# Optimization experiments

Hardware: AMD Instinct MI355X
Metric: run time of the kernel (lower is better)

The kernel has to match this reference:

```python
import jax, jax.numpy as jnp
import numpy as np

B, H = 65536, 1024


def setup_inputs() -> dict:
    key = jax.random.key(0)
    ks = jax.random.split(key, 8)
    pos = jax.random.normal(ks[0], (B, 3), dtype=jnp.float32)
    quat = jax.random.normal(ks[1], (B, 4), dtype=jnp.float32)
    quat = quat / jnp.linalg.norm(quat, axis=-1, keepdims=True)
    gripper = jax.random.randint(ks[2], (B, 1), 0, 2).astype(jnp.float32)
    actions = jnp.concatenate([pos, quat, gripper], axis=-1)  # (B, 8)
    return {
        "actions": actions,
        "pos_W": jax.random.normal(ks[3], (3, H), dtype=jnp.float32) * 0.02,
        "pos_b": jnp.zeros((H,), dtype=jnp.float32),
        "rot_W": jax.random.normal(ks[4], (6, H), dtype=jnp.float32) * 0.02,
        "rot_b": jnp.zeros((H,), dtype=jnp.float32),
        "open_emb": jax.random.normal(ks[5], (2, H), dtype=jnp.float32) * 0.02,
        "ln_g": jnp.ones((H,), dtype=jnp.float32),
        "ln_b": jnp.zeros((H,), dtype=jnp.float32),
    }


def quat_to_euler_xyz(quat):
    # scipy R.from_quat uses (x, y, z, w); as_euler('xyz') = extrinsic x-y-z
    # (classic roll/pitch/yaw). Normalize like scipy does.
    quat = quat / jnp.linalg.norm(quat, axis=-1, keepdims=True)
    x, y, z, w = quat[..., 0], quat[..., 1], quat[..., 2], quat[..., 3]
    roll = jnp.arctan2(2.0 * (w * x + y * z), 1.0 - 2.0 * (x * x + y * y))
    pitch = jnp.arcsin(jnp.clip(2.0 * (w * y - z * x), -1.0, 1.0))
    yaw = jnp.arctan2(2.0 * (w * z + x * y), 1.0 - 2.0 * (y * y + z * z))
    return jnp.stack([roll, pitch, yaw], axis=-1)


def reference(actions, pos_W, pos_b, rot_W, rot_b, open_emb, ln_g, ln_b):
    pos_embeds = actions[..., :3] @ pos_W + pos_b
    open_idx = actions[..., 7].astype(jnp.int32)
    open_embeds = open_emb[open_idx]
    # original detaches quats (.data.cpu()) before conversion
    eul = quat_to_euler_xyz(jax.lax.stop_gradient(actions[..., 3:7]))
    rot_inputs = jnp.concatenate([jnp.sin(eul), jnp.cos(eul)], axis=-1)  # (B, 6)
    rot_embeds = rot_inputs @ rot_W + rot_b
    h = pos_embeds + rot_embeds + open_embeds
    mu = jnp.mean(h, axis=-1, keepdims=True)
    var = jnp.mean(jnp.square(h - mu), axis=-1, keepdims=True)
    return (h - mu) / jnp.sqrt(var + 1e-12) * ln_g + ln_b
```

## Files before the change

kernel.cpp:

```cpp
#include <hip/hip_runtime.h>
#include <math.h>


#define HDIM  1024
#define TPB   256
#define CPT   4
#define RPB   32
#define BATCH 4

typedef float v4f __attribute__((ext_vector_type(4)));

__global__ __launch_bounds__(TPB, 4) void action_embed_kernel(
    const float* __restrict__ actions,
    const float* __restrict__ pos_W, const float* __restrict__ pos_b,
    const float* __restrict__ rot_W, const float* __restrict__ rot_b,
    const float* __restrict__ open_emb,
    const float* __restrict__ ln_g, const float* __restrict__ ln_b,
    float* __restrict__ out, int B)
{
    __shared__ float s_coef[RPB][10];
    __shared__ float s_red[2][BATCH][4][2];

    const int tid  = threadIdx.x;
    const int col  = tid * CPT;
    const int row0 = blockIdx.x * RPB;

    const float4 wp0 = *(const float4*)(pos_W + 0 * HDIM + col);
    const float4 wp1 = *(const float4*)(pos_W + 1 * HDIM + col);
    const float4 wp2 = *(const float4*)(pos_W + 2 * HDIM + col);
    const float4 wr0 = *(const float4*)(rot_W + 0 * HDIM + col);
    const float4 wr1 = *(const float4*)(rot_W + 1 * HDIM + col);
    const float4 wr2 = *(const float4*)(rot_W + 2 * HDIM + col);
    const float4 wr3 = *(const float4*)(rot_W + 3 * HDIM + col);
    const float4 wr4 = *(const float4*)(rot_W + 4 * HDIM + col);
    const float4 wr5 = *(const float4*)(rot_W + 5 * HDIM + col);
    float4 bb, dopen;
    {
        const float4 pb = *(const float4*)(pos_b + col);
        const float4 rb = *(const float4*)(rot_b + col);
        const float4 o0 = *(const float4*)(open_emb + 0 * HDIM + col);
        const float4 o1 = *(const float4*)(open_emb + 1 * HDIM + col);
        bb    = make_float4(pb.x + rb.x + o0.x, pb.y + rb.y + o0.y,
                            pb.z + rb.z + o0.z, pb.w + rb.w + o0.w);
        dopen = make_float4(o1.x - o0.x, o1.y - o0.y, o1.z - o0.z, o1.w - o0.w);
    }
    const float4 g  = *(const float4*)(ln_g + col);
    const float4 bt = *(const float4*)(ln_b + col);

    if (tid < RPB) {
        const int r = row0 + tid;
        if (r < B) {
            const float4 a0 = *(const float4*)(actions + (size_t)r * 8);
            const float4 a1 = *(const float4*)(actions + (size_t)r * 8 + 4);
            float qx = a0.w, qy = a1.x, qz = a1.y, qw = a1.z;
            const float n = 1.0f / sqrtf(qx * qx + qy * qy + qz * qz + qw * qw);
            qx *= n; qy *= n; qz *= n; qw *= n;
            const float sr_n = 2.0f * (qw * qx + qy * qz);
            const float cr_n = 1.0f - 2.0f * (qx * qx + qy * qy);
            float sr, cr;
            {
                const float r2 = sr_n * sr_n + cr_n * cr_n;
                if (r2 < 1e-37f) { sr = 0.0f; cr = 1.0f; }
                else { const float ri = 1.0f / sqrtf(r2); sr = sr_n * ri; cr = cr_n * ri; }
            }
            float sp = 2.0f * (qw * qy - qz * qx);
            sp = fminf(1.0f, fmaxf(-1.0f, sp));
            const float cp = sqrtf(fmaxf(0.0f, 1.0f - sp * sp));
            const float sy_n = 2.0f * (qw * qz + qx * qy);
            const float cy_n = 1.0f - 2.0f * (qy * qy + qz * qz);
            float sy, cy;
            {
                const float r2 = sy_n * sy_n + cy_n * cy_n;
                if (r2 < 1e-37f) { sy = 0.0f; cy = 1.0f; }
                else { const float ri = 1.0f / sqrtf(r2); sy = sy_n * ri; cy = cy_n * ri; }
            }
            s_coef[tid][0] = a0.x;
            s_coef[tid][1] = a0.y;
            s_coef[tid][2] = a0.z;
            s_coef[tid][3] = sr;
            s_coef[tid][4] = sp;
            s_coef[tid][5] = sy;
            s_coef[tid][6] = cr;
            s_coef[tid][7] = cp;
            s_coef[tid][8] = cy;
            int idx = (int)a1.w;
            idx = idx < 0 ? 0 : (idx > 1 ? 1 : idx);
            s_coef[tid][9] = (float)idx;
        }
    }
    __syncthreads();

    const int wave = tid >> 6;
    const int lane = tid & 63;
    const int nrows = (B - row0 < RPB) ? (B - row0) : RPB;

    for (int rb = 0; rb < nrows; rb += BATCH) {
        const int buf = (rb >> 2) & 1;
        float4 h[BATCH];
        float  ps[BATCH], pq[BATCH];

        #pragma unroll
        for (int j = 0; j < BATCH; ++j) {
            const int rr = rb + j;
            const float c0 = s_coef[rr][0], c1 = s_coef[rr][1], c2 = s_coef[rr][2];
            const float sr = s_coef[rr][3], sp = s_coef[rr][4], sy = s_coef[rr][5];
            const float cr = s_coef[rr][6], cp = s_coef[rr][7], cy = s_coef[rr][8];
            const float op = s_coef[rr][9];
#define COMPONENT(f)                                                        \
            {                                                               \
                float hh = fmaf(op, dopen.f, bb.f);                         \
                hh = fmaf(c0, wp0.f, hh);                                   \
                hh = fmaf(c1, wp1.f, hh);                                   \
                hh = fmaf(c2, wp2.f, hh);                                   \
                hh = fmaf(sr, wr0.f, hh);                                   \
                hh = fmaf(sp, wr1.f, hh);                                   \
                hh = fmaf(sy, wr2.f, hh);                                   \
                hh = fmaf(cr, wr3.f, hh);                                   \
                hh = fmaf(cp, wr4.f, hh);                                   \
                hh = fmaf(cy, wr5.f, hh);                                   \
                h[j].f = hh;                                                \
            }
            COMPONENT(x) COMPONENT(y) COMPONENT(z) COMPONENT(w)
#undef COMPONENT
            ps[j] = (h[j].x + h[j].y) + (h[j].z + h[j].w);
            float q = h[j].x * h[j].x;
            q = fmaf(h[j].y, h[j].y, q);
            q = fmaf(h[j].z, h[j].z, q);
            q = fmaf(h[j].w, h[j].w, q);
            pq[j] = q;
        }

        #pragma unroll
        for (int off = 32; off > 0; off >>= 1) {
            #pragma unroll
            for (int j = 0; j < BATCH; ++j) {
                ps[j] += __shfl_xor(ps[j], off, 64);
                pq[j] += __shfl_xor(pq[j], off, 64);
            }
        }
        if (lane == 0) {
            #pragma unroll
            for (int j = 0; j < BATCH; ++j) {
                s_red[buf][j][wave][0] = ps[j];
                s_red[buf][j][wave][1] = pq[j];
            }
        }
        __syncthreads();

        #pragma unroll
        for (int j = 0; j < BATCH; ++j) {
            const float4 p0 = *(const float4*)&s_red[buf][j][0][0];
            const float4 p1 = *(const float4*)&s_red[buf][j][2][0];
            const float sum = (p0.x + p0.z) + (p1.x + p1.z);
            const float sq  = (p0.y + p0.w) + (p1.y + p1.w);
            const float mu  = sum * (1.0f / HDIM);
            float var = fmaf(sq, 1.0f / HDIM, -mu * mu);
            var = fmaxf(var, 0.0f);
            const float rstd = 1.0f / sqrtf(var + 1e-12f);

            v4f o;
            o.x = fmaf((h[j].x - mu) * rstd, g.x, bt.x);
            o.y = fmaf((h[j].y - mu) * rstd, g.y, bt.y);
            o.z = fmaf((h[j].z - mu) * rstd, g.z, bt.z);
            o.w = fmaf((h[j].w - mu) * rstd, g.w, bt.w);
            __builtin_nontemporal_store(o,
                (v4f*)(out + (size_t)(row0 + rb + j) * HDIM + col));
        }
    }
}

extern "C" void kernel_launch(void* const* d_in, const int* in_sizes, int n_in,
                              void* d_out, int out_size, void* d_ws, size_t ws_size,
                              hipStream_t stream) {
    const float* actions  = (const float*)d_in[0];
    const float* pos_W    = (const float*)d_in[1];
    const float* pos_b    = (const float*)d_in[2];
    const float* rot_W    = (const float*)d_in[3];
    const float* rot_b    = (const float*)d_in[4];
    const float* open_emb = (const float*)d_in[5];
    const float* ln_g     = (const float*)d_in[6];
    const float* ln_b     = (const float*)d_in[7];
    float* out = (float*)d_out;

    const int B = in_sizes[0] / 8;
    const int grid = (B + RPB - 1) / RPB;
    hipLaunchKernelGGL(action_embed_kernel, dim3(grid), dim3(TPB), 0, stream,
                       actions, pos_W, pos_b, rot_W, rot_b, open_emb,
                       ln_g, ln_b, out, B);
}
```

Measured before the change: 296.0 us.

## Compute LayerNorm statistics analytically via precomputed Gram matrix of basis vectors

Adds a small pre-kernel that computes the 11x11 Gram matrix and column sums of the weight/bias basis vectors into workspace. Each row's mean and variance then come from a quadratic form of its 11 coefficients, so the per-row cross-wave reductions and block barriers in the main loop go away. Coefficients are prescaled by rstd, which leaves a plain FMA chain followed by the store. It adds a second kernel launch and per-row serial quadratic-form work on 32 threads. Computing variance as E[h^2]-mu^2 from the Gram matrix can lose precision through cancellation.

Measured after the change: 288.7 us. 1.03x faster.

```diff
diff --git a/kernel.cpp b/kernel.cpp
--- a/kernel.cpp
+++ b/kernel.cpp
@@ -6,9 +6,56 @@
 #define TPB   256
 #define CPT   4
 #define RPB   32
-#define BATCH 4
+#define NB    11
 
 typedef float v4f __attribute__((ext_vector_type(4)));
+
+__device__ __forceinline__ float basis_val(
+    int k, int c,
+    const float* __restrict__ pos_W, const float* __restrict__ pos_b,
+    const float* __restrict__ rot_W, const float* __restrict__ rot_b,
+    const float* __restrict__ open_emb)
+{
+    if (k < 3)  return pos_W[k * HDIM + c];
+    if (k < 9)  return rot_W[(k - 3) * HDIM + c];
+    if (k == 9) return open_emb[HDIM + c] - open_emb[c];
+    return pos_b[c] + rot_b[c] + open_emb[c];
+}
+
+__global__ __launch_bounds__(TPB) void gram_kernel(
+    const float* __restrict__ pos_W, const float* __restrict__ pos_b,
+    const float* __restrict__ rot_W, const float* __restrict__ rot_b,
+    const float* __restrict__ open_emb, float* __restrict__ ws)
+{
+    __shared__ float s_part[4];
+    const int b   = blockIdx.x;
+    const int tid = threadIdx.x;
+    float acc = 0.0f;
+    if (b < NB * NB) {
+        const int k = b / NB, l = b % NB;
+        #pragma unroll
+        for (int i = 0; i < HDIM / TPB; ++i) {
+            const int c = tid + i * TPB;
+            acc = fmaf(basis_val(k, c, pos_W, pos_b, rot_W, rot_b, open_emb),
+                       basis_val(l, c, pos_W, pos_b, rot_W, rot_b, open_emb),
+                       acc);
+        }
+    } else {
+        const int k = b - NB * NB;
+        #pragma unroll
+        for (int i = 0; i < HDIM / TPB; ++i) {
+            const int c = tid + i * TPB;
+            acc += basis_val(k, c, pos_W, pos_b, rot_W, rot_b, open_emb);
+        }
+    }
+    #pragma unroll
+    for (int off = 32; off > 0; off >>= 1)
+        acc += __shfl_xor(acc, off, 64);
+    if ((tid & 63) == 0) s_part[tid >> 6] = acc;
+    __syncthreads();
+    if (tid == 0)
+        ws[b] = (s_part[0] + s_part[1]) + (s_part[2] + s_part[3]);
+}
 
 __global__ __launch_bounds__(TPB, 4) void action_embed_kernel(
     const float* __restrict__ actions,
@@ -16,10 +63,10 @@
     const float* __restrict__ rot_W, const float* __restrict__ rot_b,
     const float* __restrict__ open_emb,
     const float* __restrict__ ln_g, const float* __restrict__ ln_b,
+    const float* __restrict__ ws,
     float* __restrict__ out, int B)
 {
-    __shared__ float s_coef[RPB][10];
-    __shared__ float s_red[2][BATCH][4][2];
+    __shared__ float s_coef[RPB][12];
 
     const int tid  = threadIdx.x;
     const int col  = tid * CPT;
@@ -74,98 +121,70 @@
                 if (r2 < 1e-37f) { sy = 0.0f; cy = 1.0f; }
                 else { const float ri = 1.0f / sqrtf(r2); sy = sy_n * ri; cy = cy_n * ri; }
             }
-            s_coef[tid][0] = a0.x;
-            s_coef[tid][1] = a0.y;
-            s_coef[tid][2] = a0.z;
-            s_coef[tid][3] = sr;
-            s_coef[tid][4] = sp;
-            s_coef[tid][5] = sy;
-            s_coef[tid][6] = cr;
-            s_coef[tid][7] = cp;
-            s_coef[tid][8] = cy;
             int idx = (int)a1.w;
             idx = idx < 0 ? 0 : (idx > 1 ? 1 : idx);
-            s_coef[tid][9] = (float)idx;
-        }
-    }
-    __syncthreads();
-
-    const int wave = tid >> 6;
-    const int lane = tid & 63;
-    const int nrows = (B - row0 < RPB) ? (B - row0) : RPB;
-
-    for (int rb = 0; rb < nrows; rb += BATCH) {
-        const int buf = (rb >> 2) & 1;
-        float4 h[BATCH];
-        float  ps[BATCH], pq[BATCH];
-
-        #pragma unroll
-        for (int j = 0; j < BATCH; ++j) {
-            const int rr = rb + j;
-            const float c0 = s_coef[rr][0], c1 = s_coef[rr][1], c2 = s_coef[rr][2];
-            const float sr = s_coef[rr][3], sp = s_coef[rr][4], sy = s_coef[rr][5];
-            const float cr = s_coef[rr][6], cp = s_coef[rr][7], cy = s_coef[rr][8];
-            const float op = s_coef[rr][9];
-#define COMPONENT(f)                                                        \
-            {                                                               \
-                float hh = fmaf(op, dopen.f, bb.f);                         \
-                hh = fmaf(c0, wp0.f, hh);                                   \
-                hh = fmaf(c1, wp1.f, hh);                                   \
-                hh = fmaf(c2, wp2.f, hh);                                   \
-                hh = fmaf(sr, wr0.f, hh);                                   \
-                hh = fmaf(sp, wr1.f, hh);                                   \
-                hh = fmaf(sy, wr2.f, hh);                                   \
-                hh = fmaf(cr, wr3.f, hh);                                   \
-                hh = fmaf(cp, wr4.f, hh);                                   \
-                hh = fmaf(cy, wr5.f, hh);                                   \
-                h[j].f = hh;                                                \
+
+            float c[NB];
+            c[0] = a0.x; c[1] = a0.y; c[2] = a0.z;
+            c[3] = sr;   c[4] = sp;   c[5] = sy;
+            c[6] = cr;   c[7] = cp;   c[8] = cy;
+            c[9] = (float)idx;
+            c[10] = 1.0f;
+
+            float mdot = 0.0f;
+            #pragma unroll
+            for (int k = 0; k < NB; ++k)
+                mdot = fmaf(c[k], ws[NB * NB + k], mdot);
+            const float mu = mdot * (1.0f / HDIM);
+            float q = 0.0f;
+            #pragma unroll
+            for (int k = 0; k < NB; ++k) {
+                float t = 0.0f;
+                #pragma unroll
+                for (int l = 0; l < NB; ++l)
+                    t = fmaf(ws[k * NB + l], c[l], t);
+                q = fmaf(c[k], t, q);
             }
-            COMPONENT(x) COMPONENT(y) COMPONENT(z) COMPONENT(w)
-#undef COMPONENT
-            ps[j] = (h[j].x + h[j].y) + (h[j].z + h[j].w);
-            float q = h[j].x * h[j].x;
-            q = fmaf(h[j].y, h[j].y, q);
-            q = fmaf(h[j].z, h[j].z, q);
-            q = fmaf(h[j].w, h[j].w, q);
-            pq[j] = q;
-        }
-
-        #pragma unroll
-        for (int off = 32; off > 0; off >>= 1) {
-            #pragma unroll
-            for (int j = 0; j < BATCH; ++j) {
-                ps[j] += __shfl_xor(ps[j], off, 64);
-                pq[j] += __shfl_xor(pq[j], off, 64);
-            }
-        }
-        if (lane == 0) {
-            #pragma unroll
-            for (int j = 0; j < BATCH; ++j) {
-                s_red[buf][j][wave][0] = ps[j];
-                s_red[buf][j][wave][1] = pq[j];
-            }
-        }
-        __syncthreads();
-
-        #pragma unroll
-        for (int j = 0; j < BATCH; ++j) {
-            const float4 p0 = *(const float4*)&s_red[buf][j][0][0];
-            const float4 p1 = *(const float4*)&s_red[buf][j][2][0];
-            const float sum = (p0.x + p0.z) + (p1.x + p1.z);
-            const float sq  = (p0.y + p0.w) + (p1.y + p1.w);
-            const float mu  = sum * (1.0f / HDIM);
-            float var = fmaf(sq, 1.0f / HDIM, -mu * mu);
+            float var = fmaf(q, 1.0f / HDIM, -mu * mu);
             var = fmaxf(var, 0.0f);
             const float rstd = 1.0f / sqrtf(var + 1e-12f);
 
-            v4f o;
-            o.x = fmaf((h[j].x - mu) * rstd, g.x, bt.x);
-            o.y = fmaf((h[j].y - mu) * rstd, g.y, bt.y);
-            o.z = fmaf((h[j].z - mu) * rstd, g.z, bt.z);
-            o.w = fmaf((h[j].w - mu) * rstd, g.w, bt.w);
-            __builtin_nontemporal_store(o,
-                (v4f*)(out + (size_t)(row0 + rb + j) * HDIM + col));
-        }
+            #pragma unroll
+            for (int k = 0; k < 10; ++k)
+                s_coef[tid][k] = c[k] * rstd;
+            s_coef[tid][10] = rstd;
+            s_coef[tid][11] = mu * rstd;
+        }
+    }
+    __syncthreads();
+
+    const int nrows = (B - row0 < RPB) ? (B - row0) : RPB;
+
+    for (int rr = 0; rr < nrows; ++rr) {
+        const float4 k0 = *(const float4*)&s_coef[rr][0];
+        const float4 k1 = *(const float4*)&s_coef[rr][4];
+        const float4 k2 = *(const float4*)&s_coef[rr][8];
+
+        v4f o;
+#define COMPONENT(f)                                                        \
+        {                                                                   \
+            float hh = fmaf(k2.z, bb.f, -k2.w);                             \
+            hh = fmaf(k0.x, wp0.f, hh);                                     \
+            hh = fmaf(k0.y, wp1.f, hh);                                     \
+            hh = fmaf(k0.z, wp2.f, hh);                                     \
+            hh = fmaf(k0.w, wr0.f, hh);                                     \
+            hh = fmaf(k1.x, wr1.f, hh);                                     \
+            hh = fmaf(k1.y, wr2.f, hh);                                     \
+            hh = fmaf(k1.z, wr3.f, hh);                                     \
+            hh = fmaf(k1.w, wr4.f, hh);                                     \
+            hh = fmaf(k2.x, wr5.f, hh);                                     \
+            hh = fmaf(k2.y, dopen.f, hh);                                   \
+            o.f = fmaf(hh, g.f, bt.f);                                      \
+        }
+        COMPONENT(x) COMPONENT(y) COMPONENT(z) COMPONENT(w)
+#undef COMPONENT
+        __builtin_nontemporal_store(o,
+            (v4f*)(out + (size_t)(row0 + rr) * HDIM + col));
     }
 }
 
@@ -181,10 +200,13 @@
     const float* ln_g     = (const float*)d_in[6];
     const float* ln_b     = (const float*)d_in[7];
     float* out = (float*)d_out;
+    float* ws  = (float*)d_ws;
 
     const int B = in_sizes[0] / 8;
+    hipLaunchKernelGGL(gram_kernel, dim3(NB * NB + NB), dim3(TPB), 0, stream,
+                       pos_W, pos_b, rot_W, rot_b, open_emb, ws);
     const int grid = (B + RPB - 1) / RPB;
     hipLaunchKernelGGL(action_embed_kernel, dim3(grid), dim3(TPB), 0, stream,
                        actions, pos_W, pos_b, rot_W, rot_b, open_emb,
-                       ln_g, ln_b, out, B);
-}
+                       ln_g, ln_b, ws, out, B);
+}
```
